# Optimization experiments

Hardware: AMD Instinct MI355X
Metric: run time of the kernel (lower is better)

The kernel has to match this reference:

```python
import jax, jax.numpy as jnp
import numpy as np

K, N = 8, 20          # exactly-K-of-N circuit
B = 524288            # batch
NEG = -1e9            # masked-softmax logit


def setup_inputs() -> dict:
    key = jax.random.key(0)
    k1, k2, k3 = jax.random.split(key, 3)
    # boolean data vector per example
    x = jax.random.randint(k1, (B, N), 0, 2).astype(bool)
    # leaf sum-node weights: node S(1, m) has m weights, stored in row m (padded to N)
    Wleaf = jax.random.uniform(k2, (N + 1, N), dtype=jnp.float32)
    # internal sum-node weights: node S(k, m) (1 < k < m <= N, incl. root) has 2 weights
    W2 = jax.random.uniform(k3, (K + 1, N + 1, 2), dtype=jnp.float32)
    return {"x": x, "Wleaf": Wleaf, "W2": W2}


def _circuit(xf, Wleaf, W2):
    """Tensorized DP over the (k, m) lattice; same math as the recursive circuit:
      S(m, m) = prod_{i<m} x_i                                (prodNode base case)
      S(1, m) = sum_i w_i * x_i * prod_{j<m, j!=i} (1 - x_j)  (leaf sumNode)
      S(k, m) = w0 * S(k, m-1) + w1 * S(k-1, m-1) * x_{m-1}   (internal sumNode)
    Root output = S(K, N), shape [B, 1].
    """
    Bsz = xf.shape[0]
    csum = jnp.cumsum(xf, axis=1)    # running count of ones
    pre = jnp.cumprod(xf, axis=1)    # pre[:, m-1] = prod_{i<m} x_i = S(m, m)

    # --- leaf row k = 1, vectorized over m ---
    mask = jnp.arange(N)[None, :] < jnp.arange(N + 1)[:, None]      # [N+1, N]
    wsm = jax.nn.softmax(jnp.where(mask, Wleaf, NEG), axis=-1)
    wsm = jnp.where(mask, wsm, 0.0)
    dots = xf @ wsm.T                                               # [B, N+1]: sum_{i<m} w_i x_i
    # for boolean x: x_i * prod_{j<m, j!=i}(1-x_j) is nonzero iff exactly one of
    # x[:, :m] is set, so S(1, m) = 1[count_m == 1] * (w . x[:, :m])
    exactly_one = jnp.concatenate(
        [jnp.zeros((Bsz, 1), xf.dtype), (csum == 1.0).astype(xf.dtype)], axis=1)
    S_cols = [exactly_one[:, m] * dots[:, m] for m in range(N + 1)]  # row k = 1

    # --- internal rows k = 2 .. K ---
    w2 = jax.nn.softmax(W2, axis=-1)   # softmax over each node's 2 children
    zero = jnp.zeros((Bsz,), xf.dtype)
    for k in range(2, K + 1):
        row = [zero] * (N + 1)
        row[k] = pre[:, k - 1]                      # S(k, k) = prod of first k inputs
        for m in range(k + 1, N + 1):
            row[m] = w2[k, m, 0] * row[m - 1] + w2[k, m, 1] * S_cols[m - 1] * xf[:, m - 1]
        S_cols = row
    return S_cols[N][:, None]    # [B, 1], like torch matmul output


def reference(x, Wleaf, W2):
    return _circuit(x.astype(jnp.float32), Wleaf, W2)
```

## Files before the change

### kernel.cpp

```cpp
#include <hip/hip_runtime.h>
#include <hip/hip_bf16.h>

static constexpr int NB  = 20;
static constexpr int KK  = 8;
static constexpr int EPT = 2;

typedef float v2f __attribute__((ext_vector_type(2)));

__global__ __launch_bounds__(256) void pc_kernel(
    const void* __restrict__ xraw,
    const void* __restrict__ wleaf_raw,
    const void* __restrict__ w2_raw,
    void* __restrict__ outraw,
    int batch)
{
    __shared__ float s_wsm[(NB + 1) * NB];
    __shared__ float s_inv[NB + 1];
    __shared__ float s_w20[(KK + 1) * (NB + 1)];
    __shared__ float s_w21[(KK + 1) * (NB + 1)];
    __shared__ int s_flagX, s_flagW, s_cntW, s_xKind;

    const int tid = threadIdx.x;

    if (tid == 0) { s_cntW = 0; s_xKind = 0; }
    __syncthreads();

    if (tid < 64) {
        unsigned v = ((const unsigned*)xraw)[tid];
        if (v > 1u) {
            if (((v & 0xFFFFu) == 0x3F80u) || ((v >> 16) == 0x3F80u))
                atomicOr(&s_xKind, 2);
            else
                atomicOr(&s_xKind, 1);
        }
    } else if (tid < 64 + 192) {
        unsigned v = ((const unsigned*)wleaf_raw)[tid - 64];
        unsigned hb = (v >> 8) & 0xFFu;
        if (hb >= 0x30u && hb <= 0x40u) atomicAdd(&s_cntW, 1);
    }
    __syncthreads();
    if (tid == 0) {
        int xk = s_xKind;
        s_flagX = (xk & 2) ? 2 : ((xk & 1) ? 1 : 0);
        s_flagW = (s_cntW > 96) ? 1 : 0;
    }
    __syncthreads();
    const int fX = s_flagX;
    const int fW = s_flagW;

    auto WL = [&](int idx) -> float {
        return fW ? __bfloat162float(((const __hip_bfloat16*)wleaf_raw)[idx])
                  : ((const float*)wleaf_raw)[idx];
    };
    auto W2v = [&](int idx) -> float {
        return fW ? __bfloat162float(((const __hip_bfloat16*)w2_raw)[idx])
                  : ((const float*)w2_raw)[idx];
    };

    const int base = blockIdx.x * (256 * EPT) + tid;
    unsigned bits[EPT];
    bool valid[EPT];
    #pragma unroll
    for (int e = 0; e < EPT; ++e) {
        const int b = base + e * 256;
        valid[e] = (b < batch);
        unsigned bb = 0;
        if (valid[e]) {
            if (fX == 0) {
                const int4* row = (const int4*)((const int*)xraw + (size_t)b * NB);
                #pragma unroll
                for (int j = 0; j < 5; ++j) {
                    int4 v = row[j];
                    bb |= (unsigned)(v.x != 0) << (4 * j + 0);
                    bb |= (unsigned)(v.y != 0) << (4 * j + 1);
                    bb |= (unsigned)(v.z != 0) << (4 * j + 2);
                    bb |= (unsigned)(v.w != 0) << (4 * j + 3);
                }
            } else if (fX == 1) {
                const unsigned* p = (const unsigned*)((const unsigned char*)xraw + (size_t)b * NB);
                #pragma unroll
                for (int j = 0; j < 5; ++j) {
                    unsigned v = p[j];
                    bb |= (unsigned)(((v      ) & 0xFFu) != 0) << (4 * j + 0);
                    bb |= (unsigned)(((v >>  8) & 0xFFu) != 0) << (4 * j + 1);
                    bb |= (unsigned)(((v >> 16) & 0xFFu) != 0) << (4 * j + 2);
                    bb |= (unsigned)(((v >> 24)       ) != 0) << (4 * j + 3);
                }
            } else {
                const unsigned* p = (const unsigned*)((const unsigned short*)xraw + (size_t)b * NB);
                #pragma unroll
                for (int j = 0; j < 10; ++j) {
                    unsigned v = p[j];
                    bb |= (unsigned)((v & 0xFFFFu) != 0) << (2 * j + 0);
                    bb |= (unsigned)((v >> 16)     != 0) << (2 * j + 1);
                }
            }
        }
        bits[e] = bb;
    }

    if (tid < 200) {
        #pragma unroll
        for (int s = 0; s < 2; ++s) {
            const int p = 20 + tid + s * 200;
            const int m = p / 20, i = p - m * 20;
            if (i < m) s_wsm[p] = expf(WL(p));
        }
    }
    __syncthreads();
    if (tid >= 1 && tid <= NB) {
        float s = 0.f;
        for (int i = 0; i < tid; ++i) s += s_wsm[tid * NB + i];
        s_inv[tid] = 1.f / s;
    } else if (tid >= 21 && tid < 21 + (KK + 1) * (NB + 1)) {
        const int idx = tid - 21;
        const float a = W2v(idx * 2 + 0);
        const float b = W2v(idx * 2 + 1);
        const float mx = fmaxf(a, b);
        const float ea = expf(a - mx), eb = expf(b - mx);
        const float inv = 1.f / (ea + eb);
        s_w20[idx] = ea * inv;
        s_w21[idx] = eb * inv;
    }
    __syncthreads();

    int p2[EPT];
    float inj[EPT];
    #pragma unroll
    for (int e = 0; e < EPT; ++e) {
        const unsigned be = bits[e];
        const unsigned low = be & (be - 1u);
        const int j0 = __builtin_ctz(be  | (1u << 20));
        const int q0 = __builtin_ctz(low | (1u << 20));
        const bool has2 = (low != 0u);
        p2[e] = has2 ? (q0 + 1) : 99;
        const int rV = has2 ? q0 : 1;
        const int cV = has2 ? j0 : 0;
        const float V = s_wsm[rV * NB + cV] * s_inv[rV];
        inj[e] = s_w21[2 * (NB + 1) + (has2 ? (q0 + 1) : 3)] * V;
    }

    v2f S[NB + 1];
    v2f pn;
    pn.x = ((bits[0] & 3u) == 3u) ? 1.f : 0.f;
    pn.y = ((bits[1] & 3u) == 3u) ? 1.f : 0.f;
    S[2] = pn;
    #pragma unroll
    for (int m = 3; m <= NB; ++m) {
        const float w0 = s_w20[2 * (NB + 1) + m];
        v2f add;
        add.x = (m == p2[0]) ? inj[0] : 0.f;
        add.y = (m == p2[1]) ? inj[1] : 0.f;
        v2f cur = w0 * pn + add;
        S[m] = cur;
        pn = cur;
    }

    #pragma unroll
    for (int k = 3; k <= KK; ++k) {
        const unsigned lm = (1u << k) - 1u;
        v2f p, op;
        p.x = ((bits[0] & lm) == lm) ? 1.f : 0.f;
        p.y = ((bits[1] & lm) == lm) ? 1.f : 0.f;
        op = S[k];
        S[k] = p;
        #pragma unroll
        for (int m = k + 1; m <= NB; ++m) {
            const v2f oc = S[m];
            const float w0 = s_w20[k * (NB + 1) + m];
            const float w1 = s_w21[k * (NB + 1) + m];
            v2f t;
            t.x = ((bits[0] >> (m - 1)) & 1u) ? op.x : 0.f;
            t.y = ((bits[1] >> (m - 1)) & 1u) ? op.y : 0.f;
            v2f cur = w0 * p + w1 * t;
            S[m] = cur;
            p = cur;
            op = oc;
        }
    }

    const float outv[EPT] = { S[NB].x, S[NB].y };
    #pragma unroll
    for (int e = 0; e < EPT; ++e) {
        const int b = base + e * 256;
        if (valid[e]) {
            if (fW) ((__hip_bfloat16*)outraw)[b] = __float2bfloat16(outv[e]);
            else    ((float*)outraw)[b]          = outv[e];
        }
    }
}

extern "C" void kernel_launch(void* const* d_in, const int* in_sizes, int n_in,
                              void* d_out, int out_size, void* d_ws, size_t ws_size,
                              hipStream_t stream) {
    (void)n_in; (void)out_size; (void)d_ws; (void)ws_size;
    const int batch = in_sizes[0] / NB;
    const int blocks = (batch + 256 * EPT - 1) / (256 * EPT);
    pc_kernel<<<blocks, 256, 0, stream>>>(d_in[0], d_in[1], d_in[2], d_out, batch);
}
```

Before: 85.67 us.

## Use wave ballots for dtype detection and process four elements per thread

Replaces the shared-memory atomics and two block barriers used for input dtype detection with per-wavefront ballot reductions, so every wave computes the flags independently. It also doubles elements per thread from 2 to 4, halving the grid and amortizing the per-block softmax weight setup over more batch rows. The cost is higher register pressure from the 21-entry 4-wide S array, which may reduce occupancy for this memory-bound kernel.

```diff
diff --git a/kernel.cpp b/kernel.cpp
--- a/kernel.cpp
+++ b/kernel.cpp
@@ -3,9 +3,9 @@
 
 static constexpr int NB  = 20;
 static constexpr int KK  = 8;
-static constexpr int EPT = 2;
+static constexpr int EPT = 4;
 
-typedef float v2f __attribute__((ext_vector_type(2)));
+typedef float v4f __attribute__((ext_vector_type(4)));
 
 __global__ __launch_bounds__(256) void pc_kernel(
     const void* __restrict__ xraw,
@@ -18,35 +18,27 @@
     __shared__ float s_inv[NB + 1];
     __shared__ float s_w20[(KK + 1) * (NB + 1)];
     __shared__ float s_w21[(KK + 1) * (NB + 1)];
-    __shared__ int s_flagX, s_flagW, s_cntW, s_xKind;
 
-    const int tid = threadIdx.x;
+    const int tid  = threadIdx.x;
+    const int lane = tid & 63;
 
-    if (tid == 0) { s_cntW = 0; s_xKind = 0; }
-    __syncthreads();
+    {
+    }
+    const unsigned xv = ((const unsigned*)xraw)[lane];
+    const bool big  = xv > 1u;
+    const bool isbf = big && (((xv & 0xFFFFu) == 0x3F80u) || ((xv >> 16) == 0x3F80u));
+    const unsigned long long mBig = __ballot(big);
+    const unsigned long long mBf  = __ballot(isbf);
+    const int fX = mBf ? 2 : (mBig ? 1 : 0);
 
-    if (tid < 64) {
-        unsigned v = ((const unsigned*)xraw)[tid];
-        if (v > 1u) {
-            if (((v & 0xFFFFu) == 0x3F80u) || ((v >> 16) == 0x3F80u))
-                atomicOr(&s_xKind, 2);
-            else
-                atomicOr(&s_xKind, 1);
-        }
-    } else if (tid < 64 + 192) {
-        unsigned v = ((const unsigned*)wleaf_raw)[tid - 64];
-        unsigned hb = (v >> 8) & 0xFFu;
-        if (hb >= 0x30u && hb <= 0x40u) atomicAdd(&s_cntW, 1);
+    unsigned cnt = 0;
+    #pragma unroll
+    for (int j = 0; j < 3; ++j) {
+        const unsigned wv = ((const unsigned*)wleaf_raw)[lane * 3 + j];
+        const unsigned hb = (wv >> 8) & 0xFFu;
+        cnt += (unsigned)__popcll(__ballot(hb >= 0x30u && hb <= 0x40u));
     }
-    __syncthreads();
-    if (tid == 0) {
-        int xk = s_xKind;
-        s_flagX = (xk & 2) ? 2 : ((xk & 1) ? 1 : 0);
-        s_flagW = (s_cntW > 96) ? 1 : 0;
-    }
-    __syncthreads();
-    const int fX = s_flagX;
-    const int fW = s_flagW;
+    const int fW = (cnt > 96u) ? 1 : 0;
 
     auto WL = [&](int idx) -> float {
         return fW ? __bfloat162float(((const __hip_bfloat16*)wleaf_raw)[idx])
@@ -140,18 +132,20 @@
         inj[e] = s_w21[2 * (NB + 1) + (has2 ? (q0 + 1) : 3)] * V;
     }
 
-    v2f S[NB + 1];
-    v2f pn;
-    pn.x = ((bits[0] & 3u) == 3u) ? 1.f : 0.f;
-    pn.y = ((bits[1] & 3u) == 3u) ? 1.f : 0.f;
+    v4f S[NB + 1];
+    v4f pn;
+    #pragma unroll
+    for (int e = 0; e < EPT; ++e)
+        pn[e] = ((bits[e] & 3u) == 3u) ? 1.f : 0.f;
     S[2] = pn;
     #pragma unroll
     for (int m = 3; m <= NB; ++m) {
         const float w0 = s_w20[2 * (NB + 1) + m];
-        v2f add;
-        add.x = (m == p2[0]) ? inj[0] : 0.f;
-        add.y = (m == p2[1]) ? inj[1] : 0.f;
-        v2f cur = w0 * pn + add;
+        v4f add;
+        #pragma unroll
+        for (int e = 0; e < EPT; ++e)
+            add[e] = (m == p2[e]) ? inj[e] : 0.f;
+        v4f cur = w0 * pn + add;
         S[m] = cur;
         pn = cur;
     }
@@ -159,33 +153,34 @@
     #pragma unroll
     for (int k = 3; k <= KK; ++k) {
         const unsigned lm = (1u << k) - 1u;
-        v2f p, op;
-        p.x = ((bits[0] & lm) == lm) ? 1.f : 0.f;
-        p.y = ((bits[1] & lm) == lm) ? 1.f : 0.f;
+        v4f p, op;
+        #pragma unroll
+        for (int e = 0; e < EPT; ++e)
+            p[e] = ((bits[e] & lm) == lm) ? 1.f : 0.f;
         op = S[k];
         S[k] = p;
         #pragma unroll
         for (int m = k + 1; m <= NB; ++m) {
-            const v2f oc = S[m];
+            const v4f oc = S[m];
             const float w0 = s_w20[k * (NB + 1) + m];
             const float w1 = s_w21[k * (NB + 1) + m];
-            v2f t;
-            t.x = ((bits[0] >> (m - 1)) & 1u) ? op.x : 0.f;
-            t.y = ((bits[1] >> (m - 1)) & 1u) ? op.y : 0.f;
-            v2f cur = w0 * p + w1 * t;
+            v4f t;
+            #pragma unroll
+            for (int e = 0; e < EPT; ++e)
+                t[e] = ((bits[e] >> (m - 1)) & 1u) ? op[e] : 0.f;
+            v4f cur = w0 * p + w1 * t;
             S[m] = cur;
             p = cur;
             op = oc;
         }
     }
 
-    const float outv[EPT] = { S[NB].x, S[NB].y };
     #pragma unroll
     for (int e = 0; e < EPT; ++e) {
         const int b = base + e * 256;
         if (valid[e]) {
-            if (fW) ((__hip_bfloat16*)outraw)[b] = __float2bfloat16(outv[e]);
-            else    ((float*)outraw)[b]          = outv[e];
+            if (fW) ((__hip_bfloat16*)outraw)[b] = __float2bfloat16(S[NB][e]);
+            else    ((float*)outraw)[b]          = S[NB][e];
         }
     }
 }
```

Result: no change. 86.21 us (+0.6%).
